# Kernel optimization log

Measured on AMD Instinct MI355X. Metric: run time of the kernel, lower is better.

The kernel has to match this reference:

```python
import jax, jax.numpy as jnp
import numpy as np
import math

JULIA_ITERS = 64
ESCAPE_RADIUS = 2.0


def _julia_escape_times(seq_len, c_real, c_imag):
    # Positions mapped to the real segment [-2, 2]; iterate z <- z^2 + c,
    # record (first iteration index where |z| > R) / ITERS, else 1.0.
    x = jnp.linspace(-2.0, 2.0, seq_len)
    zr0 = x
    zi0 = jnp.zeros_like(x)
    escaped0 = jnp.zeros(seq_len, dtype=bool)
    et0 = jnp.ones(seq_len, dtype=x.dtype)
    r2 = ESCAPE_RADIUS * ESCAPE_RADIUS

    def step(carry, it):
        zr, zi, escaped, et = carry
        nzr = zr * zr - zi * zi + c_real
        nzi = 2.0 * zr * zi + c_imag
        # torch breaks out of the loop once escaped -> freeze z afterwards
        zr = jnp.where(escaped, zr, nzr)
        zi = jnp.where(escaped, zi, nzi)
        mag2 = zr * zr + zi * zi
        newly = jnp.logical_and(~escaped, mag2 > r2)
        et = jnp.where(newly, it.astype(et.dtype) / JULIA_ITERS, et)
        escaped = jnp.logical_or(escaped, newly)
        return (zr, zi, escaped, et), None

    (_, _, _, et), _ = jax.lax.scan(step, (zr0, zi0, escaped0, et0), jnp.arange(JULIA_ITERS))
    return et


def setup_inputs() -> dict:
    key = jax.random.key(0)
    kq, kk, kv = jax.random.split(key, 3)
    B, S, D = 4, 8192, 64
    return {
        "query": jax.random.normal(kq, (B, S, D), dtype=jnp.float32),
        "key": jax.random.normal(kk, (B, S, D), dtype=jnp.float32),
        "value": jax.random.normal(kv, (B, S, D), dtype=jnp.float32),
        "julia_c_real": jnp.float32(-0.7),
        "julia_c_imag": jnp.float32(0.27),
        "escape_scale": jnp.float32(1.0),
    }


def reference(query, key, value, julia_c_real, julia_c_imag, escape_scale):
    B, S, D = key.shape
    et = _julia_escape_times(S, julia_c_real, julia_c_imag)            # [S]
    julia_weights = jnp.exp(et * escape_scale)                          # [S]
    bias = jnp.log(julia_weights + 1e-8)                                # [S]
    scores = jnp.einsum("bqd,bkd->bqk", query, key) / math.sqrt(D)     # [B,S,S]
    scores = scores + bias[None, None, :]
    attn = jax.nn.softmax(scores, axis=-1)
    out = jnp.einsum("bqk,bkd->bqd", attn, value)                       # [B,S,D]
    return out  # squeeze(1) is a no-op for S > 1
```

## Files before the change

### kernel.cpp

```cpp
#include <hip/hip_runtime.h>
#include <math.h>

#define S_LEN 8192
#define DHEAD 64
#define NBATCH 4
#define BK 32
#define KIT 32

typedef unsigned short u16;
typedef unsigned int u32;
typedef __attribute__((ext_vector_type(8))) _Float16 half8;
typedef __attribute__((ext_vector_type(2))) __fp16 fp16x2;
typedef __attribute__((ext_vector_type(4))) float f32x4;

union HU8 { int4 i4; half8 h8; u32 w[4]; };
union H2U { fp16x2 h2; u32 w; };
union HU  { _Float16 h; u16 u; };

#if __has_builtin(__builtin_amdgcn_exp2f)
#define EXP2(x) __builtin_amdgcn_exp2f(x)
#else
#define EXP2(x) exp2f(x)
#endif

__device__ __forceinline__ u16 f2h(float f) {
    HU x; x.h = (_Float16)f; return x.u;
}
__device__ __forceinline__ u32 packh2(float a, float b) {
    H2U x; x.h2 = __builtin_amdgcn_cvt_pkrtz(a, b); return x.w;
}

__global__ void prep_kernel(const float* __restrict__ K, const float* __restrict__ V,
                            const float* crp, const float* cip, const float* scp,
                            u16* __restrict__ blob, float* __restrict__ bias2) {
    int bid = blockIdx.x, tid = threadIdx.x;
    if (bid < 1024) {
        int b = bid >> 8, t = bid & 255;
        __shared__ float Kt[32 * 64];
        __shared__ float Vt[32 * 65];
        int row = tid >> 3, c8 = (tid & 7) * 8;
        const float* ks = K + ((size_t)(b * S_LEN + t * 32 + row)) * 64 + c8;
        const float* vs = V + ((size_t)(b * S_LEN + t * 32 + row)) * 64 + c8;
        float4 ka = *(const float4*)ks, kb4 = *(const float4*)(ks + 4);
        float4 va = *(const float4*)vs, vb4 = *(const float4*)(vs + 4);
        *(float4*)&Kt[row * 64 + c8] = ka;
        *(float4*)&Kt[row * 64 + c8 + 4] = kb4;
        float* vr = &Vt[row * 65 + c8];
        vr[0] = va.x; vr[1] = va.y; vr[2] = va.z; vr[3] = va.w;
        vr[4] = vb4.x; vr[5] = vb4.y; vr[6] = vb4.z; vr[7] = vb4.w;
        __syncthreads();

        int j = tid >> 6, lane = tid & 63, low = lane & 15, h = lane >> 4;
        u16* tb = blob + ((size_t)(b * 256 + t)) * 4096;
        {
            int kt = j >> 1, ds = j & 1;
            int krow = 8 * (low >> 2) + 4 * kt + (low & 3);
            const float* src = &Kt[krow * 64 + ds * 32 + h * 8];
            u32 wds[4];
#pragma unroll
            for (int i = 0; i < 4; ++i)
                wds[i] = (u32)f2h(src[2 * i]) | ((u32)f2h(src[2 * i + 1]) << 16);
            *(int4*)(tb + j * 512 + lane * 8) = make_int4(wds[0], wds[1], wds[2], wds[3]);
        }
        {
            int col = j * 16 + low;
            u32 wds[4];
#pragma unroll
            for (int i = 0; i < 4; ++i) {
                float a = Vt[(h * 8 + 2 * i) * 65 + col];
                float c = Vt[(h * 8 + 2 * i + 1) * 65 + col];
                wds[i] = (u32)f2h(a) | ((u32)f2h(c) << 16);
            }
            *(int4*)(tb + 2048 + j * 512 + lane * 8) = make_int4(wds[0], wds[1], wds[2], wds[3]);
        }
    } else {
#pragma clang fp contract(off)
        int i = (bid - 1024) * 256 + tid;
        double cr = (double)crp[0], ci = (double)cip[0], sc = (double)scp[0];
        double step = 4.0 / (double)(S_LEN - 1);
        double x = (i == S_LEN - 1) ? 2.0 : (-2.0 + step * (double)i);
        double zr = x, zi = 0.0, et = 1.0;
        bool esc = false;
        for (int it = 0; it < 64; ++it) {
            double nzr = zr * zr - zi * zi + cr;
            double nzi = 2.0 * zr * zi + ci;
            if (!esc) { zr = nzr; zi = nzi; }
            double m2 = zr * zr + zi * zi;
            if (!esc && m2 > 4.0) { et = (double)it / 64.0; esc = true; }
        }
        double bias = log(exp(et * sc) + 1e-8);
        bias2[i] = (float)(bias * 1.4426950408889634 - 20.0);
    }
}

__global__ __launch_bounds__(256, 2)
void flash_kernel(const float* __restrict__ Q, const u16* __restrict__ blob,
                  const float* __restrict__ bias2, float* __restrict__ Out,
                  float* __restrict__ O1, float* __restrict__ LS) {
    __shared__ __align__(16) char smem[17664];

    const int tid = threadIdx.x;
    const int l = tid & 63, low = l & 15, h = l >> 4;
    const int kq = __builtin_amdgcn_readfirstlane(tid >> 6);

    const int bid = blockIdx.x;
    const int batch = bid & 3;
    const int khalf = (bid >> 2) & 1;
    const int qtile = bid >> 3;
    const int q0 = qtile * 64;

    const float qscale = 0.18033688011112042f;
    half8 qfrag[4][2];
#pragma unroll
    for (int qf = 0; qf < 4; ++qf) {
        const float* qrow = Q + ((size_t)(batch * S_LEN + q0 + qf * 16 + low)) * DHEAD + h * 8;
#pragma unroll
        for (int ds = 0; ds < 2; ++ds) {
            f32x4 a = *(const f32x4*)(qrow + ds * 32);
            f32x4 b = *(const f32x4*)(qrow + ds * 32 + 4);
            HU8 u;
            u.w[0] = packh2(a[0] * qscale, a[1] * qscale);
            u.w[1] = packh2(a[2] * qscale, a[3] * qscale);
            u.w[2] = packh2(b[0] * qscale, b[1] * qscale);
            u.w[3] = packh2(b[2] * qscale, b[3] * qscale);
            qfrag[qf][ds] = u.h8;
        }
    }

    const u16* kvb = blob + ((size_t)(batch * 256 + khalf * 128 + kq * KIT)) * 4096;
    const int loff = l * 8;
    const float* bbase = bias2 + khalf * 4096 + kq * (KIT * 32);

    f32x4 o[4][4];
#pragma unroll
    for (int qf = 0; qf < 4; ++qf)
#pragma unroll
        for (int dt = 0; dt < 4; ++dt) o[qf][dt] = (f32x4){0, 0, 0, 0};
    float lsum[4] = {0.f, 0.f, 0.f, 0.f};

    HU8 kf[2][4];
    f32x4 bvv[2][2];
    HU8 vf[2][4];
    HU8 pf[4];

    auto QK = [&](const HU8 (&kfc)[4], const f32x4 (&bvc)[2], f32x4 (&st)[2][4]) {
#pragma unroll
        for (int kt = 0; kt < 2; ++kt) {
            const f32x4 binit = bvc[kt];
#pragma unroll
            for (int qf = 0; qf < 4; ++qf) {
                f32x4 a = __builtin_amdgcn_mfma_f32_16x16x32_f16(kfc[kt * 2].h8, qfrag[qf][0], binit, 0, 0, 0);
                a = __builtin_amdgcn_mfma_f32_16x16x32_f16(kfc[kt * 2 + 1].h8, qfrag[qf][1], a, 0, 0, 0);
                st[kt][qf] = a;
            }
        }
    };
    auto SM = [&](const f32x4 (&st)[2][4]) {
#pragma unroll
        for (int kt = 0; kt < 2; ++kt)
#pragma unroll
            for (int qf = 0; qf < 4; ++qf) {
                float p0 = EXP2(st[kt][qf][0]), p1 = EXP2(st[kt][qf][1]);
                float p2 = EXP2(st[kt][qf][2]), p3 = EXP2(st[kt][qf][3]);
                lsum[qf] += (p0 + p1) + (p2 + p3);
                pf[qf].w[kt * 2]     = packh2(p0, p1);
                pf[qf].w[kt * 2 + 1] = packh2(p2, p3);
            }
    };
    auto PV = [&](const HU8 (&vfc)[4]) {
#pragma unroll
        for (int dt = 0; dt < 4; ++dt)
#pragma unroll
            for (int qf = 0; qf < 4; ++qf)
                o[qf][dt] = __builtin_amdgcn_mfma_f32_16x16x32_f16(vfc[dt].h8, pf[qf].h8, o[qf][dt], 0, 0, 0);
    };

#pragma unroll
    for (int j = 0; j < 4; ++j) kf[0][j].i4 = *(const int4*)(kvb + j * 512 + loff);
    bvv[0][0] = *(const f32x4*)(bbase + h * 8);
    bvv[0][1] = *(const f32x4*)(bbase + h * 8 + 4);
#pragma unroll
    for (int j = 0; j < 4; ++j) vf[0][j].i4 = *(const int4*)(kvb + 2048 + j * 512 + loff);
#pragma unroll
    for (int j = 0; j < 4; ++j) kf[1][j].i4 = *(const int4*)(kvb + 4096 + j * 512 + loff);
    bvv[1][0] = *(const f32x4*)(bbase + 32 + h * 8);
    bvv[1][1] = *(const f32x4*)(bbase + 32 + h * 8 + 4);
    {
        f32x4 st0[2][4];
        QK(kf[0], bvv[0], st0);
        SM(st0);
    }

#define BODY(KI, C)                                                              \
    {                                                                            \
        const u16* tb_ = kvb + (size_t)(KI) * 4096;                              \
        _Pragma("unroll")                                                        \
        for (int j = 0; j < 4; ++j)                                              \
            vf[C][j].i4 = *(const int4*)(tb_ + 2048 + j * 512 + loff);           \
        _Pragma("unroll")                                                        \
        for (int j = 0; j < 4; ++j)                                              \
            kf[(C) ^ 1][j].i4 = *(const int4*)(tb_ + 4096 + j * 512 + loff);     \
        const float* bpn_ = bbase + ((KI) + 1) * 32 + h * 8;                     \
        bvv[(C) ^ 1][0] = *(const f32x4*)bpn_;                                   \
        bvv[(C) ^ 1][1] = *(const f32x4*)(bpn_ + 4);                             \
        f32x4 st_[2][4];                                                         \
        QK(kf[C], bvv[C], st_);                                                  \
        PV(vf[(C) ^ 1]);                                                         \
        SM(st_);                                                                 \
    }

#pragma unroll 1
    for (int kp = 1; kp < KIT - 1; kp += 2) {
        BODY(kp, 1)
        BODY(kp + 1, 0)
    }
    BODY(KIT - 1, 1)
    PV(vf[1]);
#undef BODY

#pragma unroll
    for (int qf = 0; qf < 4; ++qf) {
        lsum[qf] += __shfl_xor(lsum[qf], 16, 64);
        lsum[qf] += __shfl_xor(lsum[qf], 32, 64);
    }

    float* MO = (float*)smem;
    float* ML = (float*)(smem + 17408);
#pragma unroll 1
    for (int src = 1; src < 4; ++src) {
        __syncthreads();
        if (kq == src) {
#pragma unroll
            for (int qf = 0; qf < 4; ++qf) {
                const int row = qf * 16 + low;
#pragma unroll
                for (int dt = 0; dt < 4; ++dt)
                    *(f32x4*)&MO[row * 68 + dt * 16 + h * 4] = o[qf][dt];
                if (h == 0) ML[row] = lsum[qf];
            }
        }
        __syncthreads();
        if (kq == 0) {
#pragma unroll
            for (int qf = 0; qf < 4; ++qf) {
                const int row = qf * 16 + low;
#pragma unroll
                for (int dt = 0; dt < 4; ++dt) {
                    f32x4 a = *(const f32x4*)&MO[row * 68 + dt * 16 + h * 4];
#pragma unroll
                    for (int jj = 0; jj < 4; ++jj) o[qf][dt][jj] += a[jj];
                }
                lsum[qf] += ML[row];
            }
        }
    }

    if (kq == 0) {
        float* OP = khalf ? O1 : Out;
#pragma unroll
        for (int qf = 0; qf < 4; ++qf) {
            const int row = q0 + qf * 16 + low;
            float* orow = OP + ((size_t)(batch * S_LEN + row)) * DHEAD;
#pragma unroll
            for (int dt = 0; dt < 4; ++dt)
                *(f32x4*)(orow + dt * 16 + h * 4) = o[qf][dt];
            if (h == 0)
                LS[khalf * 32768 + batch * S_LEN + row] = lsum[qf];
        }
    }
}

__global__ __launch_bounds__(256)
void merge_kernel(float* __restrict__ Out, const float* __restrict__ O1,
                  const float* __restrict__ LS) {
    const int idx = blockIdx.x * 256 + threadIdx.x;
    const int rowg = idx >> 4;
    const float l0 = LS[rowg], l1 = LS[32768 + rowg];
    const float inv = 1.f / (l0 + l1);
    f32x4 a = *(const f32x4*)(Out + (size_t)idx * 4);
    f32x4 c = *(const f32x4*)(O1 + (size_t)idx * 4);
    f32x4 r;
#pragma unroll
    for (int jj = 0; jj < 4; ++jj) r[jj] = (a[jj] + c[jj]) * inv;
    *(f32x4*)(Out + (size_t)idx * 4) = r;
}

extern "C" void kernel_launch(void* const* d_in, const int* in_sizes, int n_in,
                              void* d_out, int out_size, void* d_ws, size_t ws_size,
                              hipStream_t stream) {
    const float* Q  = (const float*)d_in[0];
    const float* K  = (const float*)d_in[1];
    const float* V  = (const float*)d_in[2];
    const float* cr = (const float*)d_in[3];
    const float* ci = (const float*)d_in[4];
    const float* sc = (const float*)d_in[5];
    float* out = (float*)d_out;

    char* ws = (char*)d_ws;
    float* bias2 = (float*)ws;
    u16*   blob  = (u16*)(ws + 32768);
    float* O1    = (float*)(ws + 8429568);
    float* LS    = (float*)(ws + 16818176);

    prep_kernel<<<dim3(1056), dim3(256), 0, stream>>>(K, V, cr, ci, sc, blob, bias2);
    flash_kernel<<<dim3(1024), dim3(256), 0, stream>>>(Q, blob, bias2, out, O1, LS);
    merge_kernel<<<dim3(2048), dim3(256), 0, stream>>>(out, O1, LS);
}
```

Baseline: 157.0 us.

## Split flash block into 2 query halves x 2 key splits for higher occupancy

Each 256-thread block now splits its four waves into two query halves of 32 rows and two key splits of 64 tiles each, rather than four key splits over 64 query rows. Per-wave accumulators shrink by half, and the kernel targets 4 waves per EU instead of launch bounds of 2 blocks, aiming for more latency hiding through occupancy. The manually double-buffered software pipeline is replaced by a simple loop with single-buffer prefetch, and the cross-wave reduction shrinks to one barrier. The tradeoff is that each wave now does twice as many iterations, the K tile is reused over fewer queries, and prefetch depth is lower. The loop also prefetches one tile past its range on the last iteration, and the workspace offsets are shifted by 256 bytes, apparently to keep that overread in bounds.

```diff
diff --git a/kernel.cpp b/kernel.cpp
--- a/kernel.cpp
+++ b/kernel.cpp
@@ -5,7 +5,7 @@
 #define DHEAD 64
 #define NBATCH 4
 #define BK 32
-#define KIT 32
+#define KIT 64
 
 typedef unsigned short u16;
 typedef unsigned int u32;
@@ -93,7 +93,8 @@
     }
 }
 
-__global__ __launch_bounds__(256, 2)
+__global__ __launch_bounds__(256)
+__attribute__((amdgpu_waves_per_eu(4)))
 void flash_kernel(const float* __restrict__ Q, const u16* __restrict__ blob,
                   const float* __restrict__ bias2, float* __restrict__ Out,
                   float* __restrict__ O1, float* __restrict__ LS) {
@@ -101,18 +102,20 @@
 
     const int tid = threadIdx.x;
     const int l = tid & 63, low = l & 15, h = l >> 4;
-    const int kq = __builtin_amdgcn_readfirstlane(tid >> 6);
+    const int wid = __builtin_amdgcn_readfirstlane(tid >> 6);
+    const int qs = wid & 1;
+    const int ks = wid >> 1;
 
     const int bid = blockIdx.x;
     const int batch = bid & 3;
     const int khalf = (bid >> 2) & 1;
     const int qtile = bid >> 3;
-    const int q0 = qtile * 64;
+    const int q0 = qtile * 64 + qs * 32;
 
     const float qscale = 0.18033688011112042f;
-    half8 qfrag[4][2];
-#pragma unroll
-    for (int qf = 0; qf < 4; ++qf) {
+    half8 qfrag[2][2];
+#pragma unroll
+    for (int qf = 0; qf < 2; ++qf) {
         const float* qrow = Q + ((size_t)(batch * S_LEN + q0 + qf * 16 + low)) * DHEAD + h * 8;
 #pragma unroll
         for (int ds = 0; ds < 2; ++ds) {
@@ -127,138 +130,106 @@
         }
     }
 
-    const u16* kvb = blob + ((size_t)(batch * 256 + khalf * 128 + kq * KIT)) * 4096;
+    const u16* kvb = blob + ((size_t)(batch * 256 + khalf * 128 + ks * 64)) * 4096;
     const int loff = l * 8;
-    const float* bbase = bias2 + khalf * 4096 + kq * (KIT * 32);
-
-    f32x4 o[4][4];
-#pragma unroll
-    for (int qf = 0; qf < 4; ++qf)
+    const float* bbase = bias2 + khalf * 4096 + ks * 2048;
+
+    f32x4 o[2][4];
+#pragma unroll
+    for (int qf = 0; qf < 2; ++qf)
 #pragma unroll
         for (int dt = 0; dt < 4; ++dt) o[qf][dt] = (f32x4){0, 0, 0, 0};
-    float lsum[4] = {0.f, 0.f, 0.f, 0.f};
-
-    HU8 kf[2][4];
-    f32x4 bvv[2][2];
-    HU8 vf[2][4];
-    HU8 pf[4];
-
-    auto QK = [&](const HU8 (&kfc)[4], const f32x4 (&bvc)[2], f32x4 (&st)[2][4]) {
+    float lsum[2] = {0.f, 0.f};
+
+    HU8 kf[4];
+    f32x4 bvv[2];
+    HU8 vf[4];
+    HU8 pf[2];
+
+#pragma unroll
+    for (int j = 0; j < 4; ++j) kf[j].i4 = *(const int4*)(kvb + j * 512 + loff);
+    bvv[0] = *(const f32x4*)(bbase + h * 8);
+    bvv[1] = *(const f32x4*)(bbase + h * 8 + 4);
+#pragma unroll
+    for (int j = 0; j < 4; ++j) vf[j].i4 = *(const int4*)(kvb + 2048 + j * 512 + loff);
+
+#pragma unroll 1
+    for (int ki = 0; ki < KIT; ++ki) {
+        f32x4 st[2][2];
 #pragma unroll
         for (int kt = 0; kt < 2; ++kt) {
-            const f32x4 binit = bvc[kt];
-#pragma unroll
-            for (int qf = 0; qf < 4; ++qf) {
-                f32x4 a = __builtin_amdgcn_mfma_f32_16x16x32_f16(kfc[kt * 2].h8, qfrag[qf][0], binit, 0, 0, 0);
-                a = __builtin_amdgcn_mfma_f32_16x16x32_f16(kfc[kt * 2 + 1].h8, qfrag[qf][1], a, 0, 0, 0);
+            const f32x4 binit = kt ? bvv[1] : bvv[0];
+#pragma unroll
+            for (int qf = 0; qf < 2; ++qf) {
+                f32x4 a = __builtin_amdgcn_mfma_f32_16x16x32_f16(kf[kt * 2].h8, qfrag[qf][0], binit, 0, 0, 0);
+                a = __builtin_amdgcn_mfma_f32_16x16x32_f16(kf[kt * 2 + 1].h8, qfrag[qf][1], a, 0, 0, 0);
                 st[kt][qf] = a;
             }
         }
-    };
-    auto SM = [&](const f32x4 (&st)[2][4]) {
+
+        const u16* tn = kvb + ((size_t)ki + 1) * 4096;
+#pragma unroll
+        for (int j = 0; j < 4; ++j) kf[j].i4 = *(const int4*)(tn + j * 512 + loff);
+        const float* bpn = bbase + (ki + 1) * 32 + h * 8;
+        bvv[0] = *(const f32x4*)bpn;
+        bvv[1] = *(const f32x4*)(bpn + 4);
+
 #pragma unroll
         for (int kt = 0; kt < 2; ++kt)
 #pragma unroll
-            for (int qf = 0; qf < 4; ++qf) {
+            for (int qf = 0; qf < 2; ++qf) {
                 float p0 = EXP2(st[kt][qf][0]), p1 = EXP2(st[kt][qf][1]);
                 float p2 = EXP2(st[kt][qf][2]), p3 = EXP2(st[kt][qf][3]);
                 lsum[qf] += (p0 + p1) + (p2 + p3);
                 pf[qf].w[kt * 2]     = packh2(p0, p1);
                 pf[qf].w[kt * 2 + 1] = packh2(p2, p3);
             }
-    };
-    auto PV = [&](const HU8 (&vfc)[4]) {
+
 #pragma unroll
         for (int dt = 0; dt < 4; ++dt)
 #pragma unroll
-            for (int qf = 0; qf < 4; ++qf)
-                o[qf][dt] = __builtin_amdgcn_mfma_f32_16x16x32_f16(vfc[dt].h8, pf[qf].h8, o[qf][dt], 0, 0, 0);
-    };
-
-#pragma unroll
-    for (int j = 0; j < 4; ++j) kf[0][j].i4 = *(const int4*)(kvb + j * 512 + loff);
-    bvv[0][0] = *(const f32x4*)(bbase + h * 8);
-    bvv[0][1] = *(const f32x4*)(bbase + h * 8 + 4);
-#pragma unroll
-    for (int j = 0; j < 4; ++j) vf[0][j].i4 = *(const int4*)(kvb + 2048 + j * 512 + loff);
-#pragma unroll
-    for (int j = 0; j < 4; ++j) kf[1][j].i4 = *(const int4*)(kvb + 4096 + j * 512 + loff);
-    bvv[1][0] = *(const f32x4*)(bbase + 32 + h * 8);
-    bvv[1][1] = *(const f32x4*)(bbase + 32 + h * 8 + 4);
-    {
-        f32x4 st0[2][4];
-        QK(kf[0], bvv[0], st0);
-        SM(st0);
-    }
-
-#define BODY(KI, C)                                                              \
-    {                                                                            \
-        const u16* tb_ = kvb + (size_t)(KI) * 4096;                              \
-        _Pragma("unroll")                                                        \
-        for (int j = 0; j < 4; ++j)                                              \
-            vf[C][j].i4 = *(const int4*)(tb_ + 2048 + j * 512 + loff);           \
-        _Pragma("unroll")                                                        \
-        for (int j = 0; j < 4; ++j)                                              \
-            kf[(C) ^ 1][j].i4 = *(const int4*)(tb_ + 4096 + j * 512 + loff);     \
-        const float* bpn_ = bbase + ((KI) + 1) * 32 + h * 8;                     \
-        bvv[(C) ^ 1][0] = *(const f32x4*)bpn_;                                   \
-        bvv[(C) ^ 1][1] = *(const f32x4*)(bpn_ + 4);                             \
-        f32x4 st_[2][4];                                                         \
-        QK(kf[C], bvv[C], st_);                                                  \
-        PV(vf[(C) ^ 1]);                                                         \
-        SM(st_);                                                                 \
-    }
-
-#pragma unroll 1
-    for (int kp = 1; kp < KIT - 1; kp += 2) {
-        BODY(kp, 1)
-        BODY(kp + 1, 0)
-    }
-    BODY(KIT - 1, 1)
-    PV(vf[1]);
-#undef BODY
-
-#pragma unroll
-    for (int qf = 0; qf < 4; ++qf) {
+            for (int qf = 0; qf < 2; ++qf)
+                o[qf][dt] = __builtin_amdgcn_mfma_f32_16x16x32_f16(vf[dt].h8, pf[qf].h8, o[qf][dt], 0, 0, 0);
+
+#pragma unroll
+        for (int j = 0; j < 4; ++j) vf[j].i4 = *(const int4*)(tn + 2048 + j * 512 + loff);
+    }
+
+#pragma unroll
+    for (int qf = 0; qf < 2; ++qf) {
         lsum[qf] += __shfl_xor(lsum[qf], 16, 64);
         lsum[qf] += __shfl_xor(lsum[qf], 32, 64);
     }
 
-    float* MO = (float*)smem;
-    float* ML = (float*)(smem + 17408);
-#pragma unroll 1
-    for (int src = 1; src < 4; ++src) {
-        __syncthreads();
-        if (kq == src) {
-#pragma unroll
-            for (int qf = 0; qf < 4; ++qf) {
-                const int row = qf * 16 + low;
-#pragma unroll
-                for (int dt = 0; dt < 4; ++dt)
-                    *(f32x4*)&MO[row * 68 + dt * 16 + h * 4] = o[qf][dt];
-                if (h == 0) ML[row] = lsum[qf];
-            }
-        }
-        __syncthreads();
-        if (kq == 0) {
-#pragma unroll
-            for (int qf = 0; qf < 4; ++qf) {
-                const int row = qf * 16 + low;
-#pragma unroll
-                for (int dt = 0; dt < 4; ++dt) {
-                    f32x4 a = *(const f32x4*)&MO[row * 68 + dt * 16 + h * 4];
-#pragma unroll
-                    for (int jj = 0; jj < 4; ++jj) o[qf][dt][jj] += a[jj];
-                }
-                lsum[qf] += ML[row];
-            }
-        }
-    }
-
-    if (kq == 0) {
+    float* MO = (float*)smem + qs * 2208;
+    float* ML = MO + 2176;
+    if (ks == 1) {
+#pragma unroll
+        for (int qf = 0; qf < 2; ++qf) {
+            const int row = qf * 16 + low;
+#pragma unroll
+            for (int dt = 0; dt < 4; ++dt)
+                *(f32x4*)&MO[row * 68 + dt * 16 + h * 4] = o[qf][dt];
+            if (h == 0) ML[row] = lsum[qf];
+        }
+    }
+    __syncthreads();
+    if (ks == 0) {
+#pragma unroll
+        for (int qf = 0; qf < 2; ++qf) {
+            const int row = qf * 16 + low;
+#pragma unroll
+            for (int dt = 0; dt < 4; ++dt) {
+                f32x4 a = *(const f32x4*)&MO[row * 68 + dt * 16 + h * 4];
+#pragma unroll
+                for (int jj = 0; jj < 4; ++jj) o[qf][dt][jj] += a[jj];
+            }
+            lsum[qf] += ML[row];
+        }
+
         float* OP = khalf ? O1 : Out;
 #pragma unroll
-        for (int qf = 0; qf < 4; ++qf) {
+        for (int qf = 0; qf < 2; ++qf) {
             const int row = q0 + qf * 16 + low;
             float* orow = OP + ((size_t)(batch * S_LEN + row)) * DHEAD;
 #pragma unroll
@@ -298,9 +269,9 @@
 
     char* ws = (char*)d_ws;
     float* bias2 = (float*)ws;
-    u16*   blob  = (u16*)(ws + 32768);
-    float* O1    = (float*)(ws + 8429568);
-    float* LS    = (float*)(ws + 16818176);
+    u16*   blob  = (u16*)(ws + 33024);
+    float* O1    = (float*)(ws + 8429824);
+    float* LS    = (float*)(ws + 16818432);
 
     prep_kernel<<<dim3(1056), dim3(256), 0, stream>>>(K, V, cr, ci, sc, blob, bias2);
     flash_kernel<<<dim3(1024), dim3(256), 0, stream>>>(Q, blob, bias2, out, O1, LS);
```

Result: slower. 171.5 us (+9.2%).
